# Kernel tuning notes

Hardware: AMD Instinct MI355X
Metric: run time of the kernel (lower is better)

Reference implementation:

```python
import jax, jax.numpy as jnp
import numpy as np

S, B, D, H = 2048, 2, 1024, 16
DK = D // H  # 64
SCALE = 1.0 / np.sqrt(DK)


def setup_inputs() -> dict:
    key = jax.random.key(0)
    ks = jax.random.split(key, 12)
    std = 0.02
    return {
        "query": jax.random.normal(ks[0], (S, B, D), jnp.float32),
        "key": jax.random.normal(ks[1], (S, B, D), jnp.float32),
        "value": jax.random.normal(ks[2], (S, B, D), jnp.float32),
        "wq": jax.random.normal(ks[3], (D, D), jnp.float32) * std,
        "bq": jnp.zeros((D,), jnp.float32),
        "wk": jax.random.normal(ks[4], (D, D), jnp.float32) * std,
        "bk": jnp.zeros((D,), jnp.float32),
        "wv": jax.random.normal(ks[5], (D, D), jnp.float32) * std,
        "bv": jnp.zeros((D,), jnp.float32),
        "wo": jax.random.normal(ks[6], (D, D), jnp.float32) * std,
        "bo": jnp.zeros((D,), jnp.float32),
    }


def _proj(x, w, b):
    # (s, b, d_model) -> (s, b, heads, d_k); nn.Linear uses x @ W^T + b
    y = x @ w.T + b
    return y.reshape(*x.shape[:-1], H, DK)


def reference(query, key, value, wq, bq, wk, bk, wv, bv, wo, bo):
    q = _proj(query, wq, bq)   # (s, b, h, d)
    k = _proj(key, wk, bk)
    v = _proj(value, wv, bv)
    scores = jnp.einsum("ibhd,jbhd->ijbh", q, k) * SCALE  # (s_q, s_k, b, h)
    attn = jax.nn.softmax(scores, axis=1)  # softmax over key axis (dim=1)
    # dropout is identity in eval/reference mode
    x = jnp.einsum("ijbh,jbhd->ibhd", attn, v)  # (s, b, h, d)
    x = x.reshape(S, B, D)
    return x @ wo.T + bo
```

## Files before the change

### kernel.cpp

```cpp
#include <hip/hip_runtime.h>
#include <hip/hip_bf16.h>

namespace {

constexpr int SEQ = 2048;
constexpr int NB  = 2;
constexpr int DM  = 1024;
constexpr int NHD = 16;
constexpr int DKH = 64;
constexpr int MROWS = SEQ * NB;
constexpr float SM_SCALE = 0.125f;
constexpr size_t HT = (size_t)NB * NHD * SEQ * DKH;

typedef short bf16x8 __attribute__((ext_vector_type(8)));
typedef short bf16x4 __attribute__((ext_vector_type(4)));
typedef float f32x4  __attribute__((ext_vector_type(4)));

__device__ inline short f2bf(float f) {
    __hip_bfloat16 h = __float2bfloat16(f);
    return *reinterpret_cast<short*>(&h);
}

__device__ inline void gload_lds16(const short* g, short* l) {
    __builtin_amdgcn_global_load_lds(
        (const __attribute__((address_space(1))) void*)g,
        (__attribute__((address_space(3))) void*)l, 16, 0, 0);
}

__device__ inline f32x4 mfma16x16x16(bf16x4 a, bf16x4 b, f32x4 c) {
#if __has_builtin(__builtin_amdgcn_mfma_f32_16x16x16bf16_1k)
    return __builtin_amdgcn_mfma_f32_16x16x16bf16_1k(a, b, c, 0, 0, 0);
#else
    f32x4 d;
    asm("v_mfma_f32_16x16x16_bf16 %0, %1, %2, %3"
        : "=v"(d) : "v"(a), "v"(b), "v"(c));
    return d;
#endif
}

__global__ __launch_bounds__(256)
void cast3_kernel(const float* __restrict__ q, const float* __restrict__ k,
                  const float* __restrict__ v, short* __restrict__ oq,
                  short* __restrict__ ok, short* __restrict__ ov)
{
    const int t = blockIdx.x * 256 + threadIdx.x;
    const float* s = blockIdx.y == 0 ? q : blockIdx.y == 1 ? k : v;
    short* d       = blockIdx.y == 0 ? oq : blockIdx.y == 1 ? ok : ov;
    const float4 a = ((const float4*)s)[2 * t];
    const float4 b = ((const float4*)s)[2 * t + 1];
    short r[8] = {f2bf(a.x), f2bf(a.y), f2bf(a.z), f2bf(a.w),
                  f2bf(b.x), f2bf(b.y), f2bf(b.z), f2bf(b.w)};
    *(bf16x8*)(d + 8 * (size_t)t) = *(bf16x8*)r;
}

__global__ __launch_bounds__(256)
void castW_kernel(const float* __restrict__ w0, const float* __restrict__ w1,
                  const float* __restrict__ w2, const float* __restrict__ w3,
                  short* __restrict__ o)
{
    const int t = blockIdx.x * 256 + threadIdx.x;
    const float* s = blockIdx.y == 0 ? w0 : blockIdx.y == 1 ? w1
                   : blockIdx.y == 2 ? w2 : w3;
    short* d = o + (size_t)blockIdx.y * (DM * DM);
    const float4 a = ((const float4*)s)[2 * t];
    const float4 b = ((const float4*)s)[2 * t + 1];
    short r[8] = {f2bf(a.x), f2bf(a.y), f2bf(a.z), f2bf(a.w),
                  f2bf(b.x), f2bf(b.y), f2bf(b.z), f2bf(b.w)};
    *(bf16x8*)(d + 8 * (size_t)t) = *(bf16x8*)r;
}

template <int MODE>
__global__ __launch_bounds__(256)
void gemm2(const short* __restrict__ X0, const short* __restrict__ X1,
           const short* __restrict__ X2, const short* __restrict__ W,
           const float* __restrict__ b0, const float* __restrict__ b1,
           const float* __restrict__ b2, short* __restrict__ Yh,
           float* __restrict__ Yf)
{
    __shared__ short As[128 * 64];
    __shared__ short Bs[128 * 64];
    const int tid  = threadIdx.x;
    const int lane = tid & 63;
    const int wave = tid >> 6;
    const int i16  = lane & 15;
    const int quad = lane >> 4;
    const int m0   = blockIdx.x * 128;
    const int n0g  = blockIdx.y * 128;
    const int R0   = (wave & 1) * 64;
    const int C0   = (wave >> 1) * 64;

    const int seg = (MODE == 0) ? (n0g >> 10) : 0;
    const short* X = (MODE == 0)
        ? (seg == 0 ? X0 : seg == 1 ? X1 : X2)
        : X0;

    const int srow = lane >> 3;
    const int ssl  = (lane & 7) ^ srow;

    const short* ag[4]; short* al[4];
    const short* bg[4]; short* bl[4];
    #pragma unroll
    for (int i = 0; i < 4; ++i) {
        const int row = i * 32 + wave * 8 + srow;
        ag[i] = X + (size_t)(m0 + row) * DM + ssl * 8;
        al[i] = &As[i * 2048 + wave * 512];
        bg[i] = W + (size_t)(n0g + row) * DM + ssl * 8;
        bl[i] = &Bs[i * 2048 + wave * 512];
    }

    int aoff[4][2], boff[4][2];
    #pragma unroll
    for (int rt = 0; rt < 4; ++rt)
        #pragma unroll
        for (int kc = 0; kc < 2; ++kc)
            aoff[rt][kc] = (R0 + rt * 16 + i16) * 64 +
                           (((kc * 4 + quad) ^ (i16 & 7)) * 8);
    #pragma unroll
    for (int ct = 0; ct < 4; ++ct)
        #pragma unroll
        for (int kc = 0; kc < 2; ++kc)
            boff[ct][kc] = (C0 + ct * 16 + i16) * 64 +
                           (((kc * 4 + quad) ^ (i16 & 7)) * 8);

    f32x4 acc[4][4];
    #pragma unroll
    for (int rt = 0; rt < 4; ++rt)
        #pragma unroll
        for (int ct = 0; ct < 4; ++ct) acc[rt][ct] = (f32x4){0.f, 0.f, 0.f, 0.f};

    for (int ks = 0; ks < 16; ++ks) {
        __syncthreads();
        #pragma unroll
        for (int i = 0; i < 4; ++i) gload_lds16(ag[i], al[i]);
        #pragma unroll
        for (int i = 0; i < 4; ++i) gload_lds16(bg[i], bl[i]);
        __syncthreads();

        #pragma unroll
        for (int kc = 0; kc < 2; ++kc) {
            bf16x8 af[4], bfr[4];
            #pragma unroll
            for (int rt = 0; rt < 4; ++rt) af[rt] = *(const bf16x8*)&As[aoff[rt][kc]];
            #pragma unroll
            for (int ct = 0; ct < 4; ++ct) bfr[ct] = *(const bf16x8*)&Bs[boff[ct][kc]];
            #pragma unroll
            for (int rt = 0; rt < 4; ++rt)
                #pragma unroll
                for (int ct = 0; ct < 4; ++ct)
                    acc[rt][ct] = __builtin_amdgcn_mfma_f32_16x16x32_bf16(
                        af[rt], bfr[ct], acc[rt][ct], 0, 0, 0);
        }
        #pragma unroll
        for (int i = 0; i < 4; ++i) { ag[i] += 64; bg[i] += 64; }
    }

    #pragma unroll
    for (int ct = 0; ct < 4; ++ct) {
        const int n = n0g + C0 + ct * 16 + i16;
        if (MODE == 0) {
            const int nn  = n & 1023;
            const int h = nn >> 6, dk = nn & 63;
            const float* bp = seg == 0 ? b0 : seg == 1 ? b1 : b2;
            const float bb = bp[nn];
            const float sc = seg == 0 ? SM_SCALE : 1.0f;
            short* dst = Yh + (size_t)seg * HT;
            #pragma unroll
            for (int rt = 0; rt < 4; ++rt)
                #pragma unroll
                for (int r = 0; r < 4; ++r) {
                    const int m = m0 + R0 + rt * 16 + quad * 4 + r;
                    const int s = m >> 1, b = m & 1;
                    dst[((size_t)(b * NHD + h) * SEQ + s) * DKH + dk] =
                        f2bf((acc[rt][ct][r] + bb) * sc);
                }
        } else {
            const float bb = b0[n];
            #pragma unroll
            for (int rt = 0; rt < 4; ++rt)
                #pragma unroll
                for (int r = 0; r < 4; ++r) {
                    const int m = m0 + R0 + rt * 16 + quad * 4 + r;
                    Yf[(size_t)m * DM + n] = acc[rt][ct][r] + bb;
                }
        }
    }
}

__global__ __launch_bounds__(256)
void transpose_v(const short* __restrict__ V, short* __restrict__ Vt)
{
    __shared__ alignas(16) short tile[64][72];
    const int tid = threadIdx.x;
    const int s0  = blockIdx.x * 64;
    const int bh  = blockIdx.y;
    const int row = tid >> 2;
    const int c0  = (tid & 3) * 16;

    const short* src = V + ((size_t)bh * SEQ + s0 + row) * DKH + c0;
    *(bf16x8*)&tile[row][c0]     = *(const bf16x8*)src;
    *(bf16x8*)&tile[row][c0 + 8] = *(const bf16x8*)(src + 8);
    __syncthreads();

    alignas(16) short vals[16];
    #pragma unroll
    for (int i = 0; i < 16; ++i) vals[i] = tile[c0 + i][row];
    short* dst = Vt + ((size_t)bh * DKH + row) * SEQ + s0 + c0;
    *(bf16x8*)dst       = *(bf16x8*)&vals[0];
    *(bf16x8*)(dst + 8) = *(bf16x8*)&vals[8];
}

__global__ __launch_bounds__(256)
void attn_mfma2(const short* __restrict__ Qb, const short* __restrict__ Kb,
                const short* __restrict__ Vtb, short* __restrict__ Xa)
{
    __shared__ short Ks[64 * 64];
    __shared__ short Vs[64 * 64];
    const int tid  = threadIdx.x;
    const int lane = tid & 63;
    const int wave = tid >> 6;
    const int i16  = lane & 15;
    const int quad = lane >> 4;
    const int r0   = blockIdx.x * 128;
    const int bh   = blockIdx.y;

    bf16x8 qf[2][2];
    #pragma unroll
    for (int qt = 0; qt < 2; ++qt) {
        const short* qrow =
            Qb + ((size_t)bh * SEQ + r0 + wave * 32 + qt * 16 + i16) * DKH;
        qf[qt][0] = *(const bf16x8*)(qrow + quad * 8);
        qf[qt][1] = *(const bf16x8*)(qrow + 32 + quad * 8);
    }

    f32x4 o[2][4];
    #pragma unroll
    for (int qt = 0; qt < 2; ++qt)
        #pragma unroll
        for (int dkt = 0; dkt < 4; ++dkt) o[qt][dkt] = (f32x4){0.f, 0.f, 0.f, 0.f};
    float lsum[2] = {0.f, 0.f};

    const int srow = lane >> 3;
    const int ssl  = (lane & 7) ^ srow;
    const short* kg[2]; short* kl[2];
    const short* vg[2]; short* vl[2];
    #pragma unroll
    for (int i = 0; i < 2; ++i) {
        const int row = i * 32 + wave * 8 + srow;
        kg[i] = Kb  + (size_t)bh * SEQ * DKH + (size_t)row * DKH + ssl * 8;
        kl[i] = &Ks[i * 2048 + wave * 512];
        vg[i] = Vtb + (size_t)bh * DKH * SEQ + (size_t)row * SEQ + ssl * 8;
        vl[i] = &Vs[i * 2048 + wave * 512];
    }

    int koff[4][2];
    #pragma unroll
    for (int t = 0; t < 4; ++t)
        #pragma unroll
        for (int kc = 0; kc < 2; ++kc)
            koff[t][kc] = (t * 16 + i16) * 64 +
                          (((kc * 4 + quad) ^ (i16 & 7)) * 8);
    int voff[4][4];
    #pragma unroll
    for (int jw = 0; jw < 4; ++jw)
        #pragma unroll
        for (int dkt = 0; dkt < 4; ++dkt)
            voff[jw][dkt] = (dkt * 16 + i16) * 64 +
                            (((2 * jw + (quad >> 1)) ^ (i16 & 7)) * 8) +
                            (quad & 1) * 4;

    for (int j0 = 0; j0 < SEQ; j0 += 64) {
        __syncthreads();
        gload_lds16(kg[0] + (size_t)j0 * DKH, kl[0]);
        gload_lds16(kg[1] + (size_t)j0 * DKH, kl[1]);
        gload_lds16(vg[0] + j0, vl[0]);
        gload_lds16(vg[1] + j0, vl[1]);
        __syncthreads();

        bf16x8 kf[4][2];
        #pragma unroll
        for (int t = 0; t < 4; ++t) {
            kf[t][0] = *(const bf16x8*)&Ks[koff[t][0]];
            kf[t][1] = *(const bf16x8*)&Ks[koff[t][1]];
        }

        bf16x4 pa[2][4];
        #pragma unroll
        for (int qt = 0; qt < 2; ++qt) {
            #pragma unroll
            for (int t = 0; t < 4; ++t) {
                f32x4 st = (f32x4){0.f, 0.f, 0.f, 0.f};
                st = __builtin_amdgcn_mfma_f32_16x16x32_bf16(kf[t][0], qf[qt][0], st, 0, 0, 0);
                st = __builtin_amdgcn_mfma_f32_16x16x32_bf16(kf[t][1], qf[qt][1], st, 0, 0, 0);
                const float e0 = __expf(st[0]);
                const float e1 = __expf(st[1]);
                const float e2 = __expf(st[2]);
                const float e3 = __expf(st[3]);
                lsum[qt] += (e0 + e1) + (e2 + e3);
                bf16x4 pv;
                pv[0] = f2bf(e0); pv[1] = f2bf(e1);
                pv[2] = f2bf(e2); pv[3] = f2bf(e3);
                pa[qt][t] = pv;
            }
        }

        #pragma unroll
        for (int jw = 0; jw < 4; ++jw) {
            #pragma unroll
            for (int dkt = 0; dkt < 4; ++dkt) {
                const bf16x4 vb = *(const bf16x4*)&Vs[voff[jw][dkt]];
                o[0][dkt] = mfma16x16x16(pa[0][jw], vb, o[0][dkt]);
                o[1][dkt] = mfma16x16x16(pa[1][jw], vb, o[1][dkt]);
            }
        }
    }

    float linv[2];
    #pragma unroll
    for (int qt = 0; qt < 2; ++qt) {
        float v = lsum[qt];
        v += __shfl_xor(v, 16, 64);
        v += __shfl_xor(v, 32, 64);
        linv[qt] = 1.f / v;
    }

    const int b = bh / NHD;
    const int h = bh % NHD;
    #pragma unroll
    for (int qt = 0; qt < 2; ++qt) {
        #pragma unroll
        for (int r = 0; r < 4; ++r) {
            const float iv = __shfl(linv[qt], quad * 4 + r, 64);
            const int s = r0 + wave * 32 + qt * 16 + quad * 4 + r;
            const int m = s * NB + b;
            short* op = Xa + (size_t)m * DM + h * DKH;
            #pragma unroll
            for (int dkt = 0; dkt < 4; ++dkt)
                op[dkt * 16 + i16] = f2bf(o[qt][dkt][r] * iv);
        }
    }
}

}

extern "C" void kernel_launch(void* const* d_in, const int* in_sizes, int n_in,
                              void* d_out, int out_size, void* d_ws, size_t ws_size,
                              hipStream_t stream)
{
    const float* query = (const float*)d_in[0];
    const float* key_  = (const float*)d_in[1];
    const float* value = (const float*)d_in[2];
    const float* wq    = (const float*)d_in[3];
    const float* bq    = (const float*)d_in[4];
    const float* wk    = (const float*)d_in[5];
    const float* bk    = (const float*)d_in[6];
    const float* wv    = (const float*)d_in[7];
    const float* bv    = (const float*)d_in[8];
    const float* wo    = (const float*)d_in[9];
    const float* bo    = (const float*)d_in[10];
    float* out = (float*)d_out;

    char* ws = (char*)d_ws;
    const size_t HB = HT * sizeof(short);
    short* Qb = (short*)(ws);
    short* Kb = Qb + HT;
    short* Vb = Qb + 2 * HT;
    short* Xq = (short*)(ws + 3 * HB);
    short* Vt = Xq;
    short* Xk = (short*)(ws + 4 * HB);
    short* Xa = Xk;
    short* Xv = (short*)(ws + 5 * HB);
    short* Wb = (short*)(ws + 6 * HB);

    cast3_kernel<<<dim3(MROWS * DM / (8 * 256), 3), 256, 0, stream>>>(
        query, key_, value, Xq, Xk, Xv);
    castW_kernel<<<dim3(DM * DM / (8 * 256), 4), 256, 0, stream>>>(
        wq, wk, wv, wo, Wb);

    gemm2<0><<<dim3(MROWS / 128, 3 * DM / 128), 256, 0, stream>>>(
        Xq, Xk, Xv, Wb, bq, bk, bv, Qb, nullptr);

    transpose_v<<<dim3(SEQ / 64, NB * NHD), 256, 0, stream>>>(Vb, Vt);

    attn_mfma2<<<dim3(SEQ / 128, NB * NHD), 256, 0, stream>>>(Qb, Kb, Vt, Xa);

    gemm2<1><<<dim3(MROWS / 128, DM / 128), 256, 0, stream>>>(
        Xa, nullptr, nullptr, Wb + 3 * (size_t)DM * DM, bo, nullptr, nullptr,
        nullptr, out);
}
```

Before: 237.5 us.

## Split attention key range across two wave groups and narrow output GEMM tiles

```diff
diff --git a/kernel.cpp b/kernel.cpp
--- a/kernel.cpp
+++ b/kernel.cpp
@@ -69,13 +69,11 @@
     *(bf16x8*)(d + 8 * (size_t)t) = *(bf16x8*)r;
 }
 
-template <int MODE>
 __global__ __launch_bounds__(256)
-void gemm2(const short* __restrict__ X0, const short* __restrict__ X1,
-           const short* __restrict__ X2, const short* __restrict__ W,
-           const float* __restrict__ b0, const float* __restrict__ b1,
-           const float* __restrict__ b2, short* __restrict__ Yh,
-           float* __restrict__ Yf)
+void gemm_qkv(const short* __restrict__ X0, const short* __restrict__ X1,
+              const short* __restrict__ X2, const short* __restrict__ W,
+              const float* __restrict__ b0, const float* __restrict__ b1,
+              const float* __restrict__ b2, short* __restrict__ Yh)
 {
     __shared__ short As[128 * 64];
     __shared__ short Bs[128 * 64];
@@ -89,10 +87,8 @@
     const int R0   = (wave & 1) * 64;
     const int C0   = (wave >> 1) * 64;
 
-    const int seg = (MODE == 0) ? (n0g >> 10) : 0;
-    const short* X = (MODE == 0)
-        ? (seg == 0 ? X0 : seg == 1 ? X1 : X2)
-        : X0;
+    const int seg = n0g >> 10;
+    const short* X = seg == 0 ? X0 : seg == 1 ? X1 : X2;
 
     const int srow = lane >> 3;
     const int ssl  = (lane & 7) ^ srow;
@@ -157,32 +153,116 @@
     #pragma unroll
     for (int ct = 0; ct < 4; ++ct) {
         const int n = n0g + C0 + ct * 16 + i16;
-        if (MODE == 0) {
-            const int nn  = n & 1023;
-            const int h = nn >> 6, dk = nn & 63;
-            const float* bp = seg == 0 ? b0 : seg == 1 ? b1 : b2;
-            const float bb = bp[nn];
-            const float sc = seg == 0 ? SM_SCALE : 1.0f;
-            short* dst = Yh + (size_t)seg * HT;
-            #pragma unroll
-            for (int rt = 0; rt < 4; ++rt)
+        const int nn  = n & 1023;
+        const int h = nn >> 6, dk = nn & 63;
+        const float* bp = seg == 0 ? b0 : seg == 1 ? b1 : b2;
+        const float bb = bp[nn];
+        const float sc = seg == 0 ? SM_SCALE : 1.0f;
+        short* dst = Yh + (size_t)seg * HT;
+        #pragma unroll
+        for (int rt = 0; rt < 4; ++rt)
+            #pragma unroll
+            for (int r = 0; r < 4; ++r) {
+                const int m = m0 + R0 + rt * 16 + quad * 4 + r;
+                const int s = m >> 1, b = m & 1;
+                dst[((size_t)(b * NHD + h) * SEQ + s) * DKH + dk] =
+                    f2bf((acc[rt][ct][r] + bb) * sc);
+            }
+    }
+}
+
+__global__ __launch_bounds__(256)
+void gemm_out(const short* __restrict__ X, const short* __restrict__ W,
+              const float* __restrict__ bias, float* __restrict__ Y)
+{
+    __shared__ short As[128 * 64];
+    __shared__ short Bs[64 * 64];
+    const int tid  = threadIdx.x;
+    const int lane = tid & 63;
+    const int wave = tid >> 6;
+    const int i16  = lane & 15;
+    const int quad = lane >> 4;
+    const int m0   = blockIdx.x * 128;
+    const int n0   = blockIdx.y * 64;
+    const int R0   = wave * 32;
+
+    const int srow = lane >> 3;
+    const int ssl  = (lane & 7) ^ srow;
+
+    const short* ag[4]; short* al[4];
+    const short* bg[2]; short* bl[2];
+    #pragma unroll
+    for (int i = 0; i < 4; ++i) {
+        const int row = i * 32 + wave * 8 + srow;
+        ag[i] = X + (size_t)(m0 + row) * DM + ssl * 8;
+        al[i] = &As[i * 2048 + wave * 512];
+    }
+    #pragma unroll
+    for (int i = 0; i < 2; ++i) {
+        const int row = i * 32 + wave * 8 + srow;
+        bg[i] = W + (size_t)(n0 + row) * DM + ssl * 8;
+        bl[i] = &Bs[i * 2048 + wave * 512];
+    }
+
+    int aoff[2][2], boff[4][2];
+    #pragma unroll
+    for (int rt = 0; rt < 2; ++rt)
+        #pragma unroll
+        for (int kc = 0; kc < 2; ++kc)
+            aoff[rt][kc] = (R0 + rt * 16 + i16) * 64 +
+                           (((kc * 4 + quad) ^ (i16 & 7)) * 8);
+    #pragma unroll
+    for (int ct = 0; ct < 4; ++ct)
+        #pragma unroll
+        for (int kc = 0; kc < 2; ++kc)
+            boff[ct][kc] = (ct * 16 + i16) * 64 +
+                           (((kc * 4 + quad) ^ (i16 & 7)) * 8);
+
+    f32x4 acc[2][4];
+    #pragma unroll
+    for (int rt = 0; rt < 2; ++rt)
+        #pragma unroll
+        for (int ct = 0; ct < 4; ++ct) acc[rt][ct] = (f32x4){0.f, 0.f, 0.f, 0.f};
+
+    for (int ks = 0; ks < 16; ++ks) {
+        __syncthreads();
+        #pragma unroll
+        for (int i = 0; i < 4; ++i) gload_lds16(ag[i], al[i]);
+        #pragma unroll
+        for (int i = 0; i < 2; ++i) gload_lds16(bg[i], bl[i]);
+        __syncthreads();
+
+        #pragma unroll
+        for (int kc = 0; kc < 2; ++kc) {
+            bf16x8 af[2], bfr[4];
+            #pragma unroll
+            for (int rt = 0; rt < 2; ++rt) af[rt] = *(const bf16x8*)&As[aoff[rt][kc]];
+            #pragma unroll
+            for (int ct = 0; ct < 4; ++ct) bfr[ct] = *(const bf16x8*)&Bs[boff[ct][kc]];
+            #pragma unroll
+            for (int rt = 0; rt < 2; ++rt)
                 #pragma unroll
-                for (int r = 0; r < 4; ++r) {
-                    const int m = m0 + R0 + rt * 16 + quad * 4 + r;
-                    const int s = m >> 1, b = m & 1;
-                    dst[((size_t)(b * NHD + h) * SEQ + s) * DKH + dk] =
-                        f2bf((acc[rt][ct][r] + bb) * sc);
-                }
-        } else {
-            const float bb = b0[n];
-            #pragma unroll
-            for (int rt = 0; rt < 4; ++rt)
-                #pragma unroll
-                for (int r = 0; r < 4; ++r) {
-                    const int m = m0 + R0 + rt * 16 + quad * 4 + r;
-                    Yf[(size_t)m * DM + n] = acc[rt][ct][r] + bb;
-                }
-        }
+                for (int ct = 0; ct < 4; ++ct)
+                    acc[rt][ct] = __builtin_amdgcn_mfma_f32_16x16x32_bf16(
+                        af[rt], bfr[ct], acc[rt][ct], 0, 0, 0);
+        }
+        #pragma unroll
+        for (int i = 0; i < 4; ++i) ag[i] += 64;
+        #pragma unroll
+        for (int i = 0; i < 2; ++i) bg[i] += 64;
+    }
+
+    #pragma unroll
+    for (int ct = 0; ct < 4; ++ct) {
+        const int n = n0 + ct * 16 + i16;
+        const float bb = bias[n];
+        #pragma unroll
+        for (int rt = 0; rt < 2; ++rt)
+            #pragma unroll
+            for (int r = 0; r < 4; ++r) {
+                const int m = m0 + R0 + rt * 16 + quad * 4 + r;
+                Y[(size_t)m * DM + n] = acc[rt][ct][r] + bb;
+            }
     }
 }
 
@@ -209,25 +289,36 @@
     *(bf16x8*)(dst + 8) = *(bf16x8*)&vals[8];
 }
 
-__global__ __launch_bounds__(256)
-void attn_mfma2(const short* __restrict__ Qb, const short* __restrict__ Kb,
+__global__ __launch_bounds__(512)
+void attn_mfma3(const short* __restrict__ Qb, const short* __restrict__ Kb,
                 const short* __restrict__ Vtb, short* __restrict__ Xa)
 {
-    __shared__ short Ks[64 * 64];
-    __shared__ short Vs[64 * 64];
+    __shared__ char smem[35328];
+    float* Of = (float*)smem;
+    float* Ls = (float*)(smem + 34816);
+
     const int tid  = threadIdx.x;
     const int lane = tid & 63;
     const int wave = tid >> 6;
+    const int half = wave >> 2;
+    const int w4   = wave & 3;
     const int i16  = lane & 15;
     const int quad = lane >> 4;
-    const int r0   = blockIdx.x * 128;
-    const int bh   = blockIdx.y;
+
+    const int c   = blockIdx.y * gridDim.x + blockIdx.x;
+    const int xcd = c & 7;
+    const int idx = c >> 3;
+    const int bh  = xcd * 4 + (idx >> 4);
+    const int r0  = (idx & 15) * 128;
+
+    short* Ks = (short*)(smem + half * 8192);
+    short* Vs = (short*)(smem + 16384 + half * 8192);
 
     bf16x8 qf[2][2];
     #pragma unroll
     for (int qt = 0; qt < 2; ++qt) {
         const short* qrow =
-            Qb + ((size_t)bh * SEQ + r0 + wave * 32 + qt * 16 + i16) * DKH;
+            Qb + ((size_t)bh * SEQ + r0 + w4 * 32 + qt * 16 + i16) * DKH;
         qf[qt][0] = *(const bf16x8*)(qrow + quad * 8);
         qf[qt][1] = *(const bf16x8*)(qrow + 32 + quad * 8);
     }
@@ -245,11 +336,13 @@
     const short* vg[2]; short* vl[2];
     #pragma unroll
     for (int i = 0; i < 2; ++i) {
-        const int row = i * 32 + wave * 8 + srow;
-        kg[i] = Kb  + (size_t)bh * SEQ * DKH + (size_t)row * DKH + ssl * 8;
-        kl[i] = &Ks[i * 2048 + wave * 512];
-        vg[i] = Vtb + (size_t)bh * DKH * SEQ + (size_t)row * SEQ + ssl * 8;
-        vl[i] = &Vs[i * 2048 + wave * 512];
+        const int row = i * 32 + w4 * 8 + srow;
+        kg[i] = Kb  + (size_t)bh * SEQ * DKH +
+                (size_t)(half * 1024 + row) * DKH + ssl * 8;
+        kl[i] = &Ks[i * 2048 + w4 * 512];
+        vg[i] = Vtb + (size_t)bh * DKH * SEQ + (size_t)row * SEQ +
+                half * 1024 + ssl * 8;
+        vl[i] = &Vs[i * 2048 + w4 * 512];
     }
 
     int koff[4][2];
@@ -268,12 +361,12 @@
                             (((2 * jw + (quad >> 1)) ^ (i16 & 7)) * 8) +
                             (quad & 1) * 4;
 
-    for (int j0 = 0; j0 < SEQ; j0 += 64) {
+    for (int jt = 0; jt < 16; ++jt) {
         __syncthreads();
-        gload_lds16(kg[0] + (size_t)j0 * DKH, kl[0]);
-        gload_lds16(kg[1] + (size_t)j0 * DKH, kl[1]);
-        gload_lds16(vg[0] + j0, vl[0]);
-        gload_lds16(vg[1] + j0, vl[1]);
+        gload_lds16(kg[0] + (size_t)jt * 64 * DKH, kl[0]);
+        gload_lds16(kg[1] + (size_t)jt * 64 * DKH, kl[1]);
+        gload_lds16(vg[0] + jt * 64, vl[0]);
+        gload_lds16(vg[1] + jt * 64, vl[1]);
         __syncthreads();
 
         bf16x8 kf[4][2];
@@ -314,28 +407,51 @@
         }
     }
 
-    float linv[2];
+    float lred[2];
     #pragma unroll
     for (int qt = 0; qt < 2; ++qt) {
         float v = lsum[qt];
         v += __shfl_xor(v, 16, 64);
         v += __shfl_xor(v, 32, 64);
-        linv[qt] = 1.f / v;
-    }
-
-    const int b = bh / NHD;
-    const int h = bh % NHD;
-    #pragma unroll
-    for (int qt = 0; qt < 2; ++qt) {
-        #pragma unroll
-        for (int r = 0; r < 4; ++r) {
-            const float iv = __shfl(linv[qt], quad * 4 + r, 64);
-            const int s = r0 + wave * 32 + qt * 16 + quad * 4 + r;
-            const int m = s * NB + b;
-            short* op = Xa + (size_t)m * DM + h * DKH;
-            #pragma unroll
-            for (int dkt = 0; dkt < 4; ++dkt)
-                op[dkt * 16 + i16] = f2bf(o[qt][dkt][r] * iv);
+        lred[qt] = v;
+    }
+
+    __syncthreads();
+    if (half == 1) {
+        #pragma unroll
+        for (int qt = 0; qt < 2; ++qt) {
+            if (quad == 0) Ls[w4 * 32 + qt * 16 + i16] = lred[qt];
+            #pragma unroll
+            for (int r = 0; r < 4; ++r) {
+                const int row = w4 * 32 + qt * 16 + quad * 4 + r;
+                #pragma unroll
+                for (int dkt = 0; dkt < 4; ++dkt)
+                    Of[row * 68 + dkt * 16 + i16] = o[qt][dkt][r];
+            }
+        }
+    }
+    __syncthreads();
+    if (half == 0) {
+        const int b = bh / NHD;
+        const int h = bh % NHD;
+        float linv[2];
+        #pragma unroll
+        for (int qt = 0; qt < 2; ++qt)
+            linv[qt] = 1.f / (lred[qt] + Ls[w4 * 32 + qt * 16 + i16]);
+        #pragma unroll
+        for (int qt = 0; qt < 2; ++qt) {
+            #pragma unroll
+            for (int r = 0; r < 4; ++r) {
+                const float iv = __shfl(linv[qt], quad * 4 + r, 64);
+                const int row = w4 * 32 + qt * 16 + quad * 4 + r;
+                const int s = r0 + row;
+                const int m = s * NB + b;
+                short* op = Xa + (size_t)m * DM + h * DKH;
+                #pragma unroll
+                for (int dkt = 0; dkt < 4; ++dkt)
+                    op[dkt * 16 + i16] =
+                        f2bf((o[qt][dkt][r] + Of[row * 68 + dkt * 16 + i16]) * iv);
+            }
         }
     }
 }
@@ -376,14 +492,13 @@
     castW_kernel<<<dim3(DM * DM / (8 * 256), 4), 256, 0, stream>>>(
         wq, wk, wv, wo, Wb);
 
-    gemm2<0><<<dim3(MROWS / 128, 3 * DM / 128), 256, 0, stream>>>(
-        Xq, Xk, Xv, Wb, bq, bk, bv, Qb, nullptr);
+    gemm_qkv<<<dim3(MROWS / 128, 3 * DM / 128), 256, 0, stream>>>(
+        Xq, Xk, Xv, Wb, bq, bk, bv, Qb);
 
     transpose_v<<<dim3(SEQ / 64, NB * NHD), 256, 0, stream>>>(Vb, Vt);
 
-    attn_mfma2<<<dim3(SEQ / 128, NB * NHD), 256, 0, stream>>>(Qb, Kb, Vt, Xa);
-
-    gemm2<1><<<dim3(MROWS / 128, DM / 128), 256, 0, stream>>>(
-        Xa, nullptr, nullptr, Wb + 3 * (size_t)DM * DM, bo, nullptr, nullptr,
-        nullptr, out);
-}
+    attn_mfma3<<<dim3(SEQ / 128, NB * NHD), 512, 0, stream>>>(Qb, Kb, Vt, Xa);
+
+    gemm_out<<<dim3(MROWS / 128, DM / 64), 256, 0, stream>>>(
+        Xa, Wb + 3 * (size_t)DM * DM, bo, out);
+}
```

Measured after the change: 224.9 us. -5.3%, faster.
